# Kernel tuning notes

Hardware: AMD Instinct MI355X
Metric: run time of the kernel (lower is better)

The kernel has to match this reference:

```python
import jax, jax.numpy as jnp
import numpy as np

N_STEPS = 100
TAU_S = 5.0  # network_config['tau_s']
SHAPE = (16, 128, 16, 16, N_STEPS)  # [B, C, H, W, T]


def psp(target):
    """Leaky-integrator postsynaptic potential: syn_t = syn_{t-1}*(1-1/tau_s) + x_t, emit syn_t/tau_s."""
    x = jnp.moveaxis(target, -1, 0)  # time-major [T, B, C, H, W]
    decay = 1.0 - 1.0 / TAU_S

    def step(syn, xt):
        syn = syn * decay + xt
        return syn, syn / TAU_S

    _, syns = jax.lax.scan(step, jnp.zeros_like(x[0]), x)
    return jnp.moveaxis(syns, 0, -1)  # back to [B, C, H, W, T]


def setup_inputs() -> dict:
    key = jax.random.key(0)
    k1, k2 = jax.random.split(key)
    outputs = jax.random.normal(k1, SHAPE, dtype=jnp.float32) * 0.1
    target = (jax.random.uniform(k2, SHAPE) < 0.2).astype(jnp.float32)
    return {"outputs": outputs, "target": target}


def reference(outputs, target):
    # SpikeLoss.spike_kernel: 0.5 * sum((outputs - psp(target))**2)
    delta = outputs - psp(target)
    return 0.5 * jnp.sum(delta ** 2)
```

## Files before the change

### kernel.cpp

```cpp
#include <hip/hip_runtime.h>


#define T_STEPS 100
#define SEG 25
#define NPB 64
#define BLOCK 256
#define N_NEURONS (16 * 128 * 16 * 16)
#define GRID_P (N_NEURONS / NPB)
#define NPARTS GRID_P
#define BLK_FLOATS (NPB * T_STEPS)

#define GLOBAL_AS __attribute__((address_space(1)))
#define LDS_AS __attribute__((address_space(3)))

__device__ __forceinline__ void async_f4(const float4* g, float4* l) {
  __builtin_amdgcn_global_load_lds((const GLOBAL_AS void*)g, (LDS_AS void*)l,
                                   16, 0, 0);
}
__device__ __forceinline__ void async_f1(const float* g, float* l) {
  __builtin_amdgcn_global_load_lds((const GLOBAL_AS void*)g, (LDS_AS void*)l,
                                   4, 0, 0);
}

__device__ __forceinline__ void stage(const float* __restrict__ g,
                                      float* lds, int tid) {
  const float4* g4 = reinterpret_cast<const float4*>(g);
  float4* l4 = reinterpret_cast<float4*>(lds);
#pragma unroll
  for (int it = 0; it < 6; ++it)
    async_f4(g4 + it * BLOCK + tid, l4 + it * BLOCK + tid);
  async_f1(g + 6 * BLOCK * 4 + tid, lds + 6 * BLOCK * 4 + tid);
}

template <bool WRITE_PARTIAL>
__device__ __forceinline__ void block_body(const float* __restrict__ outputs,
                                           const float* __restrict__ target,
                                           float* __restrict__ partial,
                                           float* __restrict__ out) {
  __shared__ float buf[BLK_FLOATS];
  __shared__ float wsum[BLOCK / 64];

  const int tid = threadIdx.x;
  const size_t base = (size_t)blockIdx.x * BLK_FLOATS;

  stage(target + base, buf, tid);
  __syncthreads();

  const int s = tid & 3;
  const int rowoff = tid * SEG;
  float xr[SEG];
#pragma unroll
  for (int j = 0; j < SEG; ++j) xr[j] = buf[rowoff + j];

  __syncthreads();

  stage(outputs + base, buf, tid);

  float E = 0.f;
#pragma unroll
  for (int j = 0; j < SEG; ++j) E = fmaf(E, 0.8f, xr[j]);

  const float A25 = 3.77789319e-3f;
  const float A50 = 1.42724769e-5f;
  const float e1 = __shfl_up(E, 1, 4);
  const float e2 = __shfl_up(E, 2, 4);
  const float e3 = __shfl_up(E, 3, 4);
  float carry = 0.f;
  if (s >= 1) carry = e1;
  if (s >= 2) carry = fmaf(A25, e2, carry);
  if (s >= 3) carry = fmaf(A50, e3, carry);

  __syncthreads();

  float syn = carry;
  float acc = 0.f;
#pragma unroll
  for (int j = 0; j < SEG; ++j) {
    syn = fmaf(syn, 0.8f, xr[j]);
    float d = fmaf(-0.2f, syn, buf[rowoff + j]);
    acc = fmaf(d, d, acc);
  }

#pragma unroll
  for (int off = 32; off > 0; off >>= 1) acc += __shfl_down(acc, off, 64);
  const int lane = tid & 63;
  const int wid = tid >> 6;
  if (lane == 0) wsum[wid] = acc;
  __syncthreads();
  const float blocksum = ((wsum[0] + wsum[1]) + wsum[2]) + wsum[3];

  if (tid == 0) {
    if (WRITE_PARTIAL) partial[blockIdx.x] = blocksum;
    else atomicAdd(out, 0.5f * blocksum);
  }
}

__global__ __launch_bounds__(BLOCK, 6) void spike_loss_partial(
    const float* __restrict__ outputs,
    const float* __restrict__ target,
    float* __restrict__ partial) {
  block_body<true>(outputs, target, partial, nullptr);
}

__global__ __launch_bounds__(256) void spike_loss_final(
    const float* __restrict__ partial, float* __restrict__ out, int nparts) {
  float acc = 0.0f;
  for (int i = threadIdx.x; i < nparts; i += 256) acc += partial[i];
#pragma unroll
  for (int off = 32; off > 0; off >>= 1) acc += __shfl_down(acc, off, 64);
  __shared__ float wsum[4];
  const int lane = threadIdx.x & 63;
  const int wid = threadIdx.x >> 6;
  if (lane == 0) wsum[wid] = acc;
  __syncthreads();
  if (threadIdx.x == 0) out[0] = 0.5f * (wsum[0] + wsum[1] + wsum[2] + wsum[3]);
}

__global__ __launch_bounds__(BLOCK, 6) void spike_loss_atomic(
    const float* __restrict__ outputs,
    const float* __restrict__ target,
    float* __restrict__ out) {
  block_body<false>(outputs, target, nullptr, out);
}

extern "C" void kernel_launch(void* const* d_in, const int* in_sizes, int n_in,
                              void* d_out, int out_size, void* d_ws, size_t ws_size,
                              hipStream_t stream) {
  const float* outputs = (const float*)d_in[0];
  const float* target = (const float*)d_in[1];
  float* out = (float*)d_out;

  if (ws_size >= NPARTS * sizeof(float)) {
    float* partial = (float*)d_ws;
    spike_loss_partial<<<GRID_P, BLOCK, 0, stream>>>(outputs, target, partial);
    spike_loss_final<<<1, 256, 0, stream>>>(partial, out, NPARTS);
  } else {
    hipMemsetAsync(out, 0, sizeof(float), stream);
    spike_loss_atomic<<<GRID_P, BLOCK, 0, stream>>>(outputs, target, out);
  }
}
```

Measured before the change: 407.9 us.

## Stage both inputs concurrently through registers into separate LDS buffers

Replaces async global-to-LDS loads with register-staged float4 loads, and loads target and outputs together into two distinct LDS buffers instead of reusing one buffer sequentially. This removes two block barriers and exposes more outstanding loads per block. It doubles LDS use per block and lowers the launch-bounds occupancy hint from 6 to 3, which may reduce the number of resident blocks.

```diff
diff --git a/kernel.cpp b/kernel.cpp
--- a/kernel.cpp
+++ b/kernel.cpp
@@ -9,27 +9,26 @@
 #define GRID_P (N_NEURONS / NPB)
 #define NPARTS GRID_P
 #define BLK_FLOATS (NPB * T_STEPS)
+#define TAIL_OFF (6 * BLOCK * 4)
 
-#define GLOBAL_AS __attribute__((address_space(1)))
-#define LDS_AS __attribute__((address_space(3)))
-
-__device__ __forceinline__ void async_f4(const float4* g, float4* l) {
-  __builtin_amdgcn_global_load_lds((const GLOBAL_AS void*)g, (LDS_AS void*)l,
-                                   16, 0, 0);
-}
-__device__ __forceinline__ void async_f1(const float* g, float* l) {
-  __builtin_amdgcn_global_load_lds((const GLOBAL_AS void*)g, (LDS_AS void*)l,
-                                   4, 0, 0);
-}
-
-__device__ __forceinline__ void stage(const float* __restrict__ g,
-                                      float* lds, int tid) {
+__device__ __forceinline__ void stage_reg(const float* __restrict__ g,
+                                          float* lds, int tid) {
   const float4* g4 = reinterpret_cast<const float4*>(g);
   float4* l4 = reinterpret_cast<float4*>(lds);
-#pragma unroll
-  for (int it = 0; it < 6; ++it)
-    async_f4(g4 + it * BLOCK + tid, l4 + it * BLOCK + tid);
-  async_f1(g + 6 * BLOCK * 4 + tid, lds + 6 * BLOCK * 4 + tid);
+  float4 v0 = g4[0 * BLOCK + tid];
+  float4 v1 = g4[1 * BLOCK + tid];
+  float4 v2 = g4[2 * BLOCK + tid];
+  float4 v3 = g4[3 * BLOCK + tid];
+  float4 v4 = g4[4 * BLOCK + tid];
+  float4 v5 = g4[5 * BLOCK + tid];
+  float vt = g[TAIL_OFF + tid];
+  l4[0 * BLOCK + tid] = v0;
+  l4[1 * BLOCK + tid] = v1;
+  l4[2 * BLOCK + tid] = v2;
+  l4[3 * BLOCK + tid] = v3;
+  l4[4 * BLOCK + tid] = v4;
+  l4[5 * BLOCK + tid] = v5;
+  lds[TAIL_OFF + tid] = vt;
 }
 
 template <bool WRITE_PARTIAL>
@@ -37,24 +36,22 @@
                                            const float* __restrict__ target,
                                            float* __restrict__ partial,
                                            float* __restrict__ out) {
-  __shared__ float buf[BLK_FLOATS];
+  __shared__ float bufX[BLK_FLOATS];
+  __shared__ float bufO[BLK_FLOATS];
   __shared__ float wsum[BLOCK / 64];
 
   const int tid = threadIdx.x;
   const size_t base = (size_t)blockIdx.x * BLK_FLOATS;
 
-  stage(target + base, buf, tid);
+  stage_reg(target + base, bufX, tid);
+  stage_reg(outputs + base, bufO, tid);
   __syncthreads();
 
   const int s = tid & 3;
   const int rowoff = tid * SEG;
   float xr[SEG];
 #pragma unroll
-  for (int j = 0; j < SEG; ++j) xr[j] = buf[rowoff + j];
-
-  __syncthreads();
-
-  stage(outputs + base, buf, tid);
+  for (int j = 0; j < SEG; ++j) xr[j] = bufX[rowoff + j];
 
   float E = 0.f;
 #pragma unroll
@@ -70,14 +67,12 @@
   if (s >= 2) carry = fmaf(A25, e2, carry);
   if (s >= 3) carry = fmaf(A50, e3, carry);
 
-  __syncthreads();
-
   float syn = carry;
   float acc = 0.f;
 #pragma unroll
   for (int j = 0; j < SEG; ++j) {
     syn = fmaf(syn, 0.8f, xr[j]);
-    float d = fmaf(-0.2f, syn, buf[rowoff + j]);
+    float d = fmaf(-0.2f, syn, bufO[rowoff + j]);
     acc = fmaf(d, d, acc);
   }
 
@@ -95,7 +90,7 @@
   }
 }
 
-__global__ __launch_bounds__(BLOCK, 6) void spike_loss_partial(
+__global__ __launch_bounds__(BLOCK, 3) void spike_loss_partial(
     const float* __restrict__ outputs,
     const float* __restrict__ target,
     float* __restrict__ partial) {
@@ -116,7 +111,7 @@
   if (threadIdx.x == 0) out[0] = 0.5f * (wsum[0] + wsum[1] + wsum[2] + wsum[3]);
 }
 
-__global__ __launch_bounds__(BLOCK, 6) void spike_loss_atomic(
+__global__ __launch_bounds__(BLOCK, 3) void spike_loss_atomic(
     const float* __restrict__ outputs,
     const float* __restrict__ target,
     float* __restrict__ out) {
```

New measurement: 410.4 us. About the same (+0.6%).
